# Kernel optimization log

Measured on AMD Instinct MI355X. Metric: run time of the kernel, lower is better.

The kernel has to match this reference:

```python
import jax, jax.numpy as jnp
import numpy as np

GAMMA = 0.997
LAMDA = 0.95


def setup_inputs() -> dict:
    key = jax.random.key(0)
    k1, k2, k3, k4 = jax.random.split(key, 4)
    B, T = 131072, 64
    return {
        "predicted_continue_logits": jax.random.normal(k1, (B, T), dtype=jnp.float32),
        "rewards": jax.random.normal(k2, (B, T), dtype=jnp.float32),
        "continues": jax.random.uniform(k3, (B, T), dtype=jnp.float32),
        "critic_values": jax.random.normal(k4, (B, T), dtype=jnp.float32),
    }


def _lambda_returns(rewards, continues, values, gamma, lamda):
    # rewards/continues/values: [B, T]. Reverse-time recurrence:
    #   R_t = r_t + gamma * c_t * ((1 - lamda) * v_{t+1} + lamda * R_{t+1}),  R_{T-1} bootstrap = v_{T-1}
    r = jnp.swapaxes(rewards[:, :-1], 0, 1)    # [T-1, B]
    c = jnp.swapaxes(continues[:, :-1], 0, 1)  # [T-1, B]
    vn = jnp.swapaxes(values[:, 1:], 0, 1)     # [T-1, B] (v_{t+1})

    def step(carry, x):
        r_t, c_t, vn_t = x
        ret = r_t + gamma * c_t * ((1.0 - lamda) * vn_t + lamda * carry)
        return ret, ret

    bootstrap = values[:, -1]  # [B]
    _, rets = jax.lax.scan(step, bootstrap, (r, c, vn), reverse=True)
    return jnp.swapaxes(rets, 0, 1)  # [B, T-1]


def reference(predicted_continue_logits, rewards, continues, critic_values):
    # Bernoulli(logits).probs == sigmoid(logits)
    continue_probs = jax.nn.sigmoid(predicted_continue_logits)  # [B, T]
    lambda_returns = _lambda_returns(rewards, continues, critic_values, GAMMA, LAMDA)  # [B, T-1]
    return continue_probs, lambda_returns
```

## Files before the change

kernel.cpp:

```cpp
#include <hip/hip_runtime.h>


constexpr float GAMMA = 0.997f;
constexpr float LAMDA = 0.95f;
constexpr int T = 64;

__global__ __launch_bounds__(256) void fused_k(const float* __restrict__ logits,
                                               const float* __restrict__ rew,
                                               const float* __restrict__ con,
                                               const float* __restrict__ val,
                                               float* __restrict__ out_sig,
                                               float* __restrict__ out_ret,
                                               int B) {
  const int gid  = blockIdx.x * blockDim.x + threadIdx.x;
  const int wid  = gid >> 6;
  const int lane = gid & 63;
  const int g    = lane >> 4;
  const int q    = lane & 15;
  const int row  = wid * 4 + g;
  if (row >= B) return;

  const size_t rbase = (size_t)row * T;
  constexpr float GL  = GAMMA * LAMDA;
  constexpr float G1L = GAMMA * (1.0f - LAMDA);

  const float4 x = ((const float4*)(logits + rbase))[q];
  const float4 r = ((const float4*)(rew    + rbase))[q];
  const float4 c = ((const float4*)(con    + rbase))[q];
  const float4 v = ((const float4*)(val    + rbase))[q];
  const float v63 = val[rbase + 63];
  const float vnx = val[rbase + ((q < 15) ? 4 * q + 4 : 63)];

  float4 s;
  s.x = 1.0f / (1.0f + __expf(-x.x));
  s.y = 1.0f / (1.0f + __expf(-x.y));
  s.z = 1.0f / (1.0f + __expf(-x.z));
  s.w = 1.0f / (1.0f + __expf(-x.w));
  ((float4*)(out_sig + rbase))[q] = s;

  const float a0 = GL * c.x, b0 = fmaf(G1L * c.x, v.y, r.x);
  const float a1 = GL * c.y, b1 = fmaf(G1L * c.y, v.z, r.y);
  const float a2 = GL * c.z, b2 = fmaf(G1L * c.z, v.w, r.z);
  float a3, b3;
  if (q == 15) { a3 = 1.0f; b3 = 0.0f; }
  else         { a3 = GL * c.w; b3 = fmaf(G1L * c.w, vnx, r.w); }

  float A = a3, Bb = b3;
  A = a2 * A; Bb = fmaf(a2, Bb, b2);
  A = a1 * A; Bb = fmaf(a1, Bb, b1);
  A = a0 * A; Bb = fmaf(a0, Bb, b0);

#pragma unroll
  for (int d = 1; d < 16; d <<= 1) {
    int src = lane + d; if (src > 63) src = 63;
    float Ain = __shfl(A, src);
    float Bin = __shfl(Bb, src);
    const bool ok = (q + d) < 16;
    Ain = ok ? Ain : 1.0f;
    Bin = ok ? Bin : 0.0f;
    Bb = fmaf(A, Bin, Bb);
    A  = A * Ain;
  }

  int srcx = lane + 1; if (srcx > 63) srcx = 63;
  float Aex = __shfl(A, srcx);
  float Bex = __shfl(Bb, srcx);
  const bool okx = q < 15;
  Aex = okx ? Aex : 1.0f;
  Bex = okx ? Bex : 0.0f;
  const float carry = fmaf(Aex, v63, Bex);

  const float c3 = fmaf(a3, carry, b3);
  const float c2 = fmaf(a2, c3, b2);
  const float c1 = fmaf(a1, c2, b1);
  const float c0 = fmaf(a0, c1, b0);
  float* orow = out_ret + (size_t)row * 63 + 4 * q;
  orow[0] = c0;
  orow[1] = c1;
  orow[2] = c2;
  if (q < 15) orow[3] = c3;
}

extern "C" void kernel_launch(void* const* d_in, const int* in_sizes, int n_in,
                              void* d_out, int out_size, void* d_ws, size_t ws_size,
                              hipStream_t stream) {
  const float* logits = (const float*)d_in[0];
  const float* rew    = (const float*)d_in[1];
  const float* con    = (const float*)d_in[2];
  const float* val    = (const float*)d_in[3];
  float* out = (float*)d_out;

  const int BT = in_sizes[0];
  const int B  = BT / T;

  float* out_sig = out;
  float* out_ret = out + (size_t)BT;

  const int blocks = (B + 15) / 16;
  fused_k<<<blocks, 256, 0, stream>>>(logits, rew, con, val, out_sig, out_ret, B);
}
```

Measured before the change: 175.1 us.

## Use persistent grid-stride loop with software-prefetched next row batch

Replaces the one-row-group-per-thread launch with a fixed grid of 2048 blocks that loop over rows in a grid-stride fashion. Each iteration loads the next batch of inputs before processing and storing the current one, so memory latency overlaps compute. This cuts block launch overhead but keeps two batches live in registers, which may lower occupancy on a memory-bound streaming kernel.

```diff
diff --git a/kernel.cpp b/kernel.cpp
--- a/kernel.cpp
+++ b/kernel.cpp
@@ -5,45 +5,48 @@
 constexpr float LAMDA = 0.95f;
 constexpr int T = 64;
 
-__global__ __launch_bounds__(256) void fused_k(const float* __restrict__ logits,
-                                               const float* __restrict__ rew,
-                                               const float* __restrict__ con,
-                                               const float* __restrict__ val,
-                                               float* __restrict__ out_sig,
-                                               float* __restrict__ out_ret,
-                                               int B) {
-  const int gid  = blockIdx.x * blockDim.x + threadIdx.x;
-  const int wid  = gid >> 6;
-  const int lane = gid & 63;
-  const int g    = lane >> 4;
-  const int q    = lane & 15;
-  const int row  = wid * 4 + g;
-  if (row >= B) return;
+struct Batch {
+  float4 x, r, c, v;
+  float v63, vnx;
+};
 
+__device__ __forceinline__ Batch load_batch(const float* __restrict__ logits,
+                                            const float* __restrict__ rew,
+                                            const float* __restrict__ con,
+                                            const float* __restrict__ val,
+                                            int row, int q) {
+  const size_t rbase = (size_t)row * T;
+  Batch b;
+  b.x = ((const float4*)(logits + rbase))[q];
+  b.r = ((const float4*)(rew    + rbase))[q];
+  b.c = ((const float4*)(con    + rbase))[q];
+  b.v = ((const float4*)(val    + rbase))[q];
+  b.v63 = val[rbase + 63];
+  b.vnx = val[rbase + ((q < 15) ? 4 * q + 4 : 63)];
+  return b;
+}
+
+__device__ __forceinline__ void process_store(const Batch& bt, int row, int q,
+                                              int lane,
+                                              float* __restrict__ out_sig,
+                                              float* __restrict__ out_ret) {
   const size_t rbase = (size_t)row * T;
   constexpr float GL  = GAMMA * LAMDA;
   constexpr float G1L = GAMMA * (1.0f - LAMDA);
 
-  const float4 x = ((const float4*)(logits + rbase))[q];
-  const float4 r = ((const float4*)(rew    + rbase))[q];
-  const float4 c = ((const float4*)(con    + rbase))[q];
-  const float4 v = ((const float4*)(val    + rbase))[q];
-  const float v63 = val[rbase + 63];
-  const float vnx = val[rbase + ((q < 15) ? 4 * q + 4 : 63)];
-
   float4 s;
-  s.x = 1.0f / (1.0f + __expf(-x.x));
-  s.y = 1.0f / (1.0f + __expf(-x.y));
-  s.z = 1.0f / (1.0f + __expf(-x.z));
-  s.w = 1.0f / (1.0f + __expf(-x.w));
+  s.x = 1.0f / (1.0f + __expf(-bt.x.x));
+  s.y = 1.0f / (1.0f + __expf(-bt.x.y));
+  s.z = 1.0f / (1.0f + __expf(-bt.x.z));
+  s.w = 1.0f / (1.0f + __expf(-bt.x.w));
   ((float4*)(out_sig + rbase))[q] = s;
 
-  const float a0 = GL * c.x, b0 = fmaf(G1L * c.x, v.y, r.x);
-  const float a1 = GL * c.y, b1 = fmaf(G1L * c.y, v.z, r.y);
-  const float a2 = GL * c.z, b2 = fmaf(G1L * c.z, v.w, r.z);
+  const float a0 = GL * bt.c.x, b0 = fmaf(G1L * bt.c.x, bt.v.y, bt.r.x);
+  const float a1 = GL * bt.c.y, b1 = fmaf(G1L * bt.c.y, bt.v.z, bt.r.y);
+  const float a2 = GL * bt.c.z, b2 = fmaf(G1L * bt.c.z, bt.v.w, bt.r.z);
   float a3, b3;
   if (q == 15) { a3 = 1.0f; b3 = 0.0f; }
-  else         { a3 = GL * c.w; b3 = fmaf(G1L * c.w, vnx, r.w); }
+  else         { a3 = GL * bt.c.w; b3 = fmaf(G1L * bt.c.w, bt.vnx, bt.r.w); }
 
   float A = a3, Bb = b3;
   A = a2 * A; Bb = fmaf(a2, Bb, b2);
@@ -68,7 +71,7 @@
   const bool okx = q < 15;
   Aex = okx ? Aex : 1.0f;
   Bex = okx ? Bex : 0.0f;
-  const float carry = fmaf(Aex, v63, Bex);
+  const float carry = fmaf(Aex, bt.v63, Bex);
 
   const float c3 = fmaf(a3, carry, b3);
   const float c2 = fmaf(a2, c3, b2);
@@ -79,6 +82,37 @@
   orow[1] = c1;
   orow[2] = c2;
   if (q < 15) orow[3] = c3;
+}
+
+__global__ __launch_bounds__(256) void fused_k(const float* __restrict__ logits,
+                                               const float* __restrict__ rew,
+                                               const float* __restrict__ con,
+                                               const float* __restrict__ val,
+                                               float* __restrict__ out_sig,
+                                               float* __restrict__ out_ret,
+                                               int B) {
+  const int gid  = blockIdx.x * blockDim.x + threadIdx.x;
+  const int wid  = gid >> 6;
+  const int lane = gid & 63;
+  const int g    = lane >> 4;
+  const int q    = lane & 15;
+  const int W    = (gridDim.x * blockDim.x) >> 6;
+  const int rowstep = W * 4;
+
+  int row = wid * 4 + g;
+  if (row >= B) return;
+
+  Batch cur = load_batch(logits, rew, con, val, row, q);
+  for (;;) {
+    const int nrow = row + rowstep;
+    const bool more = (nrow < B);
+    Batch nxt;
+    if (more) nxt = load_batch(logits, rew, con, val, nrow, q);
+    process_store(cur, row, q, lane, out_sig, out_ret);
+    if (!more) break;
+    cur = nxt;
+    row = nrow;
+  }
 }
 
 extern "C" void kernel_launch(void* const* d_in, const int* in_sizes, int n_in,
@@ -96,6 +130,8 @@
   float* out_sig = out;
   float* out_ret = out + (size_t)BT;
 
-  const int blocks = (B + 15) / 16;
+  int blocks = 2048;
+  const int max_blocks = (B + 15) / 16;
+  if (blocks > max_blocks) blocks = max_blocks;
   fused_k<<<blocks, 256, 0, stream>>>(logits, rew, con, val, out_sig, out_ret, B);
 }
```

Result: slower. 180.4 us (+3.0%).
